# Performance work log

Measured on AMD Instinct MI355X. Metric: run time of the kernel, lower is better.

The kernel has to match this reference:

```python
import jax, jax.numpy as jnp
import numpy as np

TOP_K = 2


def setup_inputs() -> dict:
    key = jax.random.key(0)
    k1, k2 = jax.random.split(key)
    x = jax.random.normal(k1, (4, 4096, 2048), dtype=jnp.float32)
    W = jax.random.normal(k2, (64, 2048), dtype=jnp.float32) * (1.0 / np.sqrt(2048))
    return {"x": x, "W": W}


def reference(x, W):
    B, S, D = x.shape
    E = W.shape[0]
    # logits: [B*S, E] via linear router (no bias)
    flat = x.reshape(-1, D)
    logits = jnp.einsum('td,ed->te', flat, W)
    probs = jax.nn.softmax(logits, axis=-1)
    # eval path: top-k indices
    _, top_k_indices = jax.lax.top_k(probs, TOP_K)          # [T, K]
    # scatter 1s -> mask; scatter gathered probs -> router_probs (== probs*mask)
    router_mask = jax.nn.one_hot(top_k_indices, E, dtype=probs.dtype).sum(axis=-2)  # [T, E]
    router_probs = probs * router_mask
    # normalize (top_k > 1: gradient flows through the sum)
    router_probs = router_probs / router_probs.sum(axis=-1, keepdims=True)
    return (router_mask.reshape(B, S, E),
            top_k_indices.reshape(B, S, TOP_K),
            router_probs.reshape(B, S, E),
            probs.reshape(B, S, E))
```

## Files before the change

kernel.cpp:

```cpp
#include <hip/hip_runtime.h>
#include <math.h>


#define D_DIM 2048
#define E_DIM 64
#define KS 4
#define KSTEPS 16

typedef __bf16 bf16x8 __attribute__((ext_vector_type(8)));
typedef unsigned short us8 __attribute__((ext_vector_type(8)));
typedef float f32x4 __attribute__((ext_vector_type(4)));

#define FENCE asm volatile("" ::: "memory")

static __device__ __forceinline__ unsigned short f2bf(float f) {
    unsigned int u = __float_as_uint(f);
    u += 0x7fffu + ((u >> 16) & 1u);
    return (unsigned short)(u >> 16);
}
static __device__ __forceinline__ float bf2f(unsigned short h) {
    return __uint_as_float(((unsigned int)h) << 16);
}
static __device__ __forceinline__ void split4(const float4 v, ushort4* h, ushort4* l) {
    h->x = f2bf(v.x); l->x = f2bf(v.x - bf2f(h->x));
    h->y = f2bf(v.y); l->y = f2bf(v.y - bf2f(h->y));
    h->z = f2bf(v.z); l->z = f2bf(v.z - bf2f(h->z));
    h->w = f2bf(v.w); l->w = f2bf(v.w - bf2f(h->w));
}

static __device__ __forceinline__ void gld_lds16(const void* g, void* l) {
    __builtin_amdgcn_global_load_lds(
        (const __attribute__((address_space(1))) unsigned int*)g,
        (__attribute__((address_space(3))) unsigned int*)l,
        16, 0, 0);
}

__global__ __launch_bounds__(256, 1) void convert_w(
    const float* __restrict__ W, unsigned short* __restrict__ WB)
{
    int u = blockIdx.x * 256 + threadIdx.x;
    int lane = u & 63;
    int r = u >> 6;
    int h = r & 1;  r >>= 1;
    int n = r & 3;  int sg = r >> 2;
    int E  = n * 16 + (lane & 15);
    int k0 = sg * 32 + (lane >> 4) * 8;
    const float4* src = (const float4*)(W + (size_t)E * D_DIM + k0);
    float4 a = src[0], b = src[1];
    ushort4 ha, la, hb, lb;
    split4(a, &ha, &la);
    split4(b, &hb, &lb);
    us8 out = h ? (us8){la.x, la.y, la.z, la.w, lb.x, lb.y, lb.z, lb.w}
                : (us8){ha.x, ha.y, ha.z, ha.w, hb.x, hb.y, hb.z, hb.w};
    *(us8*)(WB + (size_t)u * 8) = out;
}

__global__ __launch_bounds__(64, 2) void gemm_part(
    const float* __restrict__ x, const unsigned short* __restrict__ WB,
    float* __restrict__ P, int T)
{
    __shared__ __align__(16) float RING[4][1024];

    const int lane = threadIdx.x;
    const int quad = lane >> 4;
    const int l16  = lane & 15;

    const int ntb = T >> 5;
    const int tb  = blockIdx.x % ntb;
    const int ksl = blockIdx.x / ntb;
    const int t0  = tb << 5;
    const int kb  = ksl * (D_DIM / KS);

    const int srow = lane >> 2;
    const int scg  = (lane & 3) ^ ((lane >> 3) & 3);

    f32x4 acc[2][4];
    #pragma unroll
    for (int g = 0; g < 2; ++g)
        #pragma unroll
        for (int n = 0; n < 4; ++n) { f32x4 z = {0.f, 0.f, 0.f, 0.f}; acc[g][n] = z; }

    auto stage = [&](int s) {
        const int kc = kb + s * 32;
        #pragma unroll
        for (int j = 0; j < 4; ++j) {
            int g = j >> 1, jj = j & 1;
            int row = g * 16 + (srow & 3) + ((srow >> 2) << 2);
            gld_lds16(x + (size_t)(t0 + row) * D_DIM + kc + jj * 16 + scg * 4,
                      &RING[s & 3][j * 256]);
        }
    };

    auto loadW = [&](int s, bf16x8 Wf[4][2]) {
        const int sg = ksl * KSTEPS + s;
        #pragma unroll
        for (int n = 0; n < 4; ++n)
            #pragma unroll
            for (int h = 0; h < 2; ++h)
                Wf[n][h] = *(const bf16x8*)(WB + ((((size_t)sg * 4 + n) * 2 + h) * 64 + lane) * 8);
    };

    bf16x8 Wc[4][2], Wn[4][2];
    stage(0);  FENCE;
    loadW(0, Wc); FENCE;
    stage(1);  FENCE;
    stage(2);  FENCE;

    const float fsw = 0.f; (void)fsw;

    #pragma unroll
    for (int s = 0; s < KSTEPS; ++s) {
        if (s + 1 < KSTEPS) loadW(s + 1, Wn);
        if (s + 3 < KSTEPS) stage(s + 3);

        if (s < 2)            asm volatile("s_waitcnt vmcnt(28)" ::: "memory");
        else if (s < KSTEPS - 3) asm volatile("s_waitcnt vmcnt(36)" ::: "memory");
        else                  asm volatile("s_waitcnt vmcnt(16)" ::: "memory");

        const int f = (l16 >> 1) & 3;
        const int jj = quad >> 1;
        const int c  = (2 * quad) & 3;
        #pragma unroll
        for (int g = 0; g < 2; ++g) {
            const float* B = &RING[s & 3][g * 512 + jj * 256];
            float4 xa = *(const float4*)&B[(l16 * 4 + ( c      ^ f)) * 4];
            float4 xb = *(const float4*)&B[(l16 * 4 + ((c + 1) ^ f)) * 4];
            ushort4 h0, l0, h1, l1;
            split4(xa, &h0, &l0);
            split4(xb, &h1, &l1);
            union { us8 u; bf16x8 b; } ua, ul;
            ua.u = (us8){h0.x, h0.y, h0.z, h0.w, h1.x, h1.y, h1.z, h1.w};
            ul.u = (us8){l0.x, l0.y, l0.z, l0.w, l1.x, l1.y, l1.z, l1.w};
            #pragma unroll
            for (int n = 0; n < 4; ++n) {
                acc[g][n] = __builtin_amdgcn_mfma_f32_16x16x32_bf16(ua.b, Wc[n][0], acc[g][n], 0, 0, 0);
                acc[g][n] = __builtin_amdgcn_mfma_f32_16x16x32_bf16(ul.b, Wc[n][0], acc[g][n], 0, 0, 0);
                acc[g][n] = __builtin_amdgcn_mfma_f32_16x16x32_bf16(ua.b, Wc[n][1], acc[g][n], 0, 0, 0);
            }
        }

        #pragma unroll
        for (int n = 0; n < 4; ++n)
            #pragma unroll
            for (int h = 0; h < 2; ++h)
                Wc[n][h] = Wn[n][h];
    }

    float* Pb = P + ((size_t)ksl * T + t0) * 64;
    #pragma unroll
    for (int g = 0; g < 2; ++g)
        #pragma unroll
        for (int n = 0; n < 4; ++n)
            #pragma unroll
            for (int r = 0; r < 4; ++r)
                Pb[(g * 16 + quad * 4 + r) * 64 + n * 16 + l16] = acc[g][n][r];
}

__global__ __launch_bounds__(256, 4) void reduce_router(
    const float* __restrict__ P, int T,
    float* __restrict__ mask_out, float* __restrict__ idx_out,
    float* __restrict__ rp_out, float* __restrict__ probs_out)
{
    const int tid  = threadIdx.x;
    const int lane = tid & 63;
    const int wv   = tid >> 6;

    for (int i = 0; i < 4; ++i) {
        int t = blockIdx.x * 16 + wv * 4 + i;
        float v = 0.f;
        #pragma unroll
        for (int s = 0; s < KS; ++s)
            v += P[((size_t)s * T + t) * 64 + lane];

        float bv = v; int bi = lane;
        #pragma unroll
        for (int off = 1; off < 64; off <<= 1) {
            float ov = __shfl_xor(bv, off, 64);
            int   oi = __shfl_xor(bi, off, 64);
            bool take = (ov > bv) || (ov == bv && oi < bi);
            bv = take ? ov : bv;
            bi = take ? oi : bi;
        }
        float m = bv; int i1 = bi;

        float p = __expf(v - m);
        float s = p;
        #pragma unroll
        for (int off = 1; off < 64; off <<= 1) s += __shfl_xor(s, off, 64);
        float prob = p / s;

        float v2 = (lane == i1) ? -INFINITY : v;
        float bv2 = v2; int bi2 = lane;
        #pragma unroll
        for (int off = 1; off < 64; off <<= 1) {
            float ov = __shfl_xor(bv2, off, 64);
            int   oi = __shfl_xor(bi2, off, 64);
            bool take = (ov > bv2) || (ov == bv2 && oi < bi2);
            bv2 = take ? ov : bv2;
            bi2 = take ? oi : bi2;
        }
        int i2 = bi2;

        float pd = __shfl(prob, i1, 64) + __shfl(prob, i2, 64);
        bool top = (lane == i1) || (lane == i2);

        mask_out[(size_t)t * 64 + lane]  = top ? 1.f : 0.f;
        rp_out[(size_t)t * 64 + lane]    = top ? prob / pd : 0.f;
        probs_out[(size_t)t * 64 + lane] = prob;
        if (lane == 0) {
            idx_out[(size_t)t * 2]     = (float)i1;
            idx_out[(size_t)t * 2 + 1] = (float)i2;
        }
    }
}

extern "C" void kernel_launch(void* const* d_in, const int* in_sizes, int n_in,
                              void* d_out, int out_size, void* d_ws, size_t ws_size,
                              hipStream_t stream) {
    const float* x = (const float*)d_in[0];
    const float* W = (const float*)d_in[1];
    float* out = (float*)d_out;

    const int T  = in_sizes[0] / D_DIM;
    const int WN = in_sizes[1];

    unsigned short* WB = (unsigned short*)d_ws;
    float* P = (float*)(WB + (size_t)WN * 2);

    float* mask_out  = out;
    float* idx_out   = out + (size_t)T * E_DIM;
    float* rp_out    = idx_out + (size_t)T * 2;
    float* probs_out = rp_out + (size_t)T * E_DIM;

    convert_w<<<dim3((WN * 2) / 8 / 256), dim3(256), 0, stream>>>(W, WB);
    gemm_part<<<dim3((T / 32) * KS), dim3(64), 0, stream>>>(x, WB, P, T);
    reduce_router<<<dim3(T / 16), dim3(256), 0, stream>>>(
        P, T, mask_out, idx_out, rp_out, probs_out);
}
```

Before: 210.0 us.

## Replace LDS ring staging with direct register loads in 4-wave blocks

The GEMM kernel drops the LDS ring buffer fed by global_load_lds and instead has each lane load its x fragments straight from global memory into registers, using a three-deep software prefetch. W fragments are double-buffered in registers. Blocks grow from one wave of 32 tokens to four waves of 16 tokens each, which reduces per-wave register pressure and raises occupancy. The change trades LDS swizzling and explicit waitcnt control for simpler loads, but each wave now reads its own W fragments, and the per-lane 32-byte x reads are strided by row, which may coalesce less well.

```diff
diff --git a/kernel.cpp b/kernel.cpp
--- a/kernel.cpp
+++ b/kernel.cpp
@@ -10,8 +10,6 @@
 typedef __bf16 bf16x8 __attribute__((ext_vector_type(8)));
 typedef unsigned short us8 __attribute__((ext_vector_type(8)));
 typedef float f32x4 __attribute__((ext_vector_type(4)));
-
-#define FENCE asm volatile("" ::: "memory")
 
 static __device__ __forceinline__ unsigned short f2bf(float f) {
     unsigned int u = __float_as_uint(f);
@@ -26,13 +24,6 @@
     h->y = f2bf(v.y); l->y = f2bf(v.y - bf2f(h->y));
     h->z = f2bf(v.z); l->z = f2bf(v.z - bf2f(h->z));
     h->w = f2bf(v.w); l->w = f2bf(v.w - bf2f(h->w));
-}
-
-static __device__ __forceinline__ void gld_lds16(const void* g, void* l) {
-    __builtin_amdgcn_global_load_lds(
-        (const __attribute__((address_space(1))) unsigned int*)g,
-        (__attribute__((address_space(3))) unsigned int*)l,
-        16, 0, 0);
 }
 
 __global__ __launch_bounds__(256, 1) void convert_w(
@@ -55,105 +46,76 @@
     *(us8*)(WB + (size_t)u * 8) = out;
 }
 
-__global__ __launch_bounds__(64, 2) void gemm_part(
+__global__ __launch_bounds__(256, 4) void gemm_part(
     const float* __restrict__ x, const unsigned short* __restrict__ WB,
     float* __restrict__ P, int T)
 {
-    __shared__ __align__(16) float RING[4][1024];
-
-    const int lane = threadIdx.x;
+    const int tid  = threadIdx.x;
+    const int lane = tid & 63;
+    const int wv   = tid >> 6;
     const int quad = lane >> 4;
     const int l16  = lane & 15;
 
-    const int ntb = T >> 5;
+    const int ntb = T >> 6;
     const int tb  = blockIdx.x % ntb;
     const int ksl = blockIdx.x / ntb;
-    const int t0  = tb << 5;
+    const int t0  = (tb << 6) + wv * 16;
     const int kb  = ksl * (D_DIM / KS);
 
-    const int srow = lane >> 2;
-    const int scg  = (lane & 3) ^ ((lane >> 3) & 3);
-
-    f32x4 acc[2][4];
-    #pragma unroll
-    for (int g = 0; g < 2; ++g)
-        #pragma unroll
-        for (int n = 0; n < 4; ++n) { f32x4 z = {0.f, 0.f, 0.f, 0.f}; acc[g][n] = z; }
-
-    auto stage = [&](int s) {
-        const int kc = kb + s * 32;
-        #pragma unroll
-        for (int j = 0; j < 4; ++j) {
-            int g = j >> 1, jj = j & 1;
-            int row = g * 16 + (srow & 3) + ((srow >> 2) << 2);
-            gld_lds16(x + (size_t)(t0 + row) * D_DIM + kc + jj * 16 + scg * 4,
-                      &RING[s & 3][j * 256]);
-        }
-    };
-
-    auto loadW = [&](int s, bf16x8 Wf[4][2]) {
-        const int sg = ksl * KSTEPS + s;
-        #pragma unroll
-        for (int n = 0; n < 4; ++n)
+    const float* xr = x + (size_t)(t0 + l16) * D_DIM + kb + quad * 8;
+    const unsigned short* wb = WB + ((size_t)(ksl * KSTEPS) * 512 + lane) * 8;
+
+    f32x4 acc[4];
+    #pragma unroll
+    for (int n = 0; n < 4; ++n) { f32x4 z = {0.f, 0.f, 0.f, 0.f}; acc[n] = z; }
+
+    float4 xa[3], xb[3];
+    bf16x8 Wf[2][4][2];
+
+    xa[0] = *(const float4*)(xr);        xb[0] = *(const float4*)(xr + 4);
+    xa[1] = *(const float4*)(xr + 32);   xb[1] = *(const float4*)(xr + 36);
+    #pragma unroll
+    for (int n = 0; n < 4; ++n)
+        #pragma unroll
+        for (int h = 0; h < 2; ++h)
+            Wf[0][n][h] = *(const bf16x8*)(wb + (n * 2 + h) * 512);
+
+    #pragma unroll
+    for (int s = 0; s < KSTEPS; ++s) {
+        if (s + 2 < KSTEPS) {
+            xa[(s + 2) % 3] = *(const float4*)(xr + (s + 2) * 32);
+            xb[(s + 2) % 3] = *(const float4*)(xr + (s + 2) * 32 + 4);
+        }
+        if (s + 1 < KSTEPS) {
             #pragma unroll
-            for (int h = 0; h < 2; ++h)
-                Wf[n][h] = *(const bf16x8*)(WB + ((((size_t)sg * 4 + n) * 2 + h) * 64 + lane) * 8);
-    };
-
-    bf16x8 Wc[4][2], Wn[4][2];
-    stage(0);  FENCE;
-    loadW(0, Wc); FENCE;
-    stage(1);  FENCE;
-    stage(2);  FENCE;
-
-    const float fsw = 0.f; (void)fsw;
-
-    #pragma unroll
-    for (int s = 0; s < KSTEPS; ++s) {
-        if (s + 1 < KSTEPS) loadW(s + 1, Wn);
-        if (s + 3 < KSTEPS) stage(s + 3);
-
-        if (s < 2)            asm volatile("s_waitcnt vmcnt(28)" ::: "memory");
-        else if (s < KSTEPS - 3) asm volatile("s_waitcnt vmcnt(36)" ::: "memory");
-        else                  asm volatile("s_waitcnt vmcnt(16)" ::: "memory");
-
-        const int f = (l16 >> 1) & 3;
-        const int jj = quad >> 1;
-        const int c  = (2 * quad) & 3;
-        #pragma unroll
-        for (int g = 0; g < 2; ++g) {
-            const float* B = &RING[s & 3][g * 512 + jj * 256];
-            float4 xa = *(const float4*)&B[(l16 * 4 + ( c      ^ f)) * 4];
-            float4 xb = *(const float4*)&B[(l16 * 4 + ((c + 1) ^ f)) * 4];
-            ushort4 h0, l0, h1, l1;
-            split4(xa, &h0, &l0);
-            split4(xb, &h1, &l1);
-            union { us8 u; bf16x8 b; } ua, ul;
-            ua.u = (us8){h0.x, h0.y, h0.z, h0.w, h1.x, h1.y, h1.z, h1.w};
-            ul.u = (us8){l0.x, l0.y, l0.z, l0.w, l1.x, l1.y, l1.z, l1.w};
-            #pragma unroll
-            for (int n = 0; n < 4; ++n) {
-                acc[g][n] = __builtin_amdgcn_mfma_f32_16x16x32_bf16(ua.b, Wc[n][0], acc[g][n], 0, 0, 0);
-                acc[g][n] = __builtin_amdgcn_mfma_f32_16x16x32_bf16(ul.b, Wc[n][0], acc[g][n], 0, 0, 0);
-                acc[g][n] = __builtin_amdgcn_mfma_f32_16x16x32_bf16(ua.b, Wc[n][1], acc[g][n], 0, 0, 0);
-            }
-        }
-
-        #pragma unroll
-        for (int n = 0; n < 4; ++n)
-            #pragma unroll
-            for (int h = 0; h < 2; ++h)
-                Wc[n][h] = Wn[n][h];
+            for (int n = 0; n < 4; ++n)
+                #pragma unroll
+                for (int h = 0; h < 2; ++h)
+                    Wf[(s + 1) & 1][n][h] =
+                        *(const bf16x8*)(wb + (size_t)(s + 1) * 4096 + (n * 2 + h) * 512);
+        }
+
+        ushort4 h0, l0, h1, l1;
+        split4(xa[s % 3], &h0, &l0);
+        split4(xb[s % 3], &h1, &l1);
+        union { us8 u; bf16x8 b; } ua, ul;
+        ua.u = (us8){h0.x, h0.y, h0.z, h0.w, h1.x, h1.y, h1.z, h1.w};
+        ul.u = (us8){l0.x, l0.y, l0.z, l0.w, l1.x, l1.y, l1.z, l1.w};
+
+        #pragma unroll
+        for (int n = 0; n < 4; ++n) {
+            acc[n] = __builtin_amdgcn_mfma_f32_16x16x32_bf16(ua.b, Wf[s & 1][n][0], acc[n], 0, 0, 0);
+            acc[n] = __builtin_amdgcn_mfma_f32_16x16x32_bf16(ul.b, Wf[s & 1][n][0], acc[n], 0, 0, 0);
+            acc[n] = __builtin_amdgcn_mfma_f32_16x16x32_bf16(ua.b, Wf[s & 1][n][1], acc[n], 0, 0, 0);
+        }
     }
 
     float* Pb = P + ((size_t)ksl * T + t0) * 64;
     #pragma unroll
-    for (int g = 0; g < 2; ++g)
-        #pragma unroll
-        for (int n = 0; n < 4; ++n)
-            #pragma unroll
-            for (int r = 0; r < 4; ++r)
-                Pb[(g * 16 + quad * 4 + r) * 64 + n * 16 + l16] = acc[g][n][r];
+    for (int n = 0; n < 4; ++n)
+        #pragma unroll
+        for (int r = 0; r < 4; ++r)
+            Pb[(quad * 4 + r) * 64 + n * 16 + l16] = acc[n][r];
 }
 
 __global__ __launch_bounds__(256, 4) void reduce_router(
@@ -233,7 +195,7 @@
     float* probs_out = rp_out + (size_t)T * E_DIM;
 
     convert_w<<<dim3((WN * 2) / 8 / 256), dim3(256), 0, stream>>>(W, WB);
-    gemm_part<<<dim3((T / 32) * KS), dim3(64), 0, stream>>>(x, WB, P, T);
+    gemm_part<<<dim3((T / 64) * KS), dim3(256), 0, stream>>>(x, WB, P, T);
     reduce_router<<<dim3(T / 16), dim3(256), 0, stream>>>(
         P, T, mask_out, idx_out, rp_out, probs_out);
 }
```

Measured after the change: 217.7 us. +3.6%, slower.
